# Kernel tuning notes

Measured on AMD Instinct MI355X. Metric: run time of the kernel, lower is better.

The kernel has to match this reference:

```python
import jax, jax.numpy as jnp
import numpy as np

EPS = 1e-5
NUM_HEADS = 8


def _ln(x, g, b):
    m = x.mean(-1, keepdims=True)
    v = jnp.mean((x - m) ** 2, -1, keepdims=True)
    return (x - m) * jax.lax.rsqrt(v + EPS) * g + b


def _bn(x, g, b, m, v):  # eval-mode BatchNorm2d on NCHW
    sh = (1, -1, 1, 1)
    return (x - m.reshape(sh)) * jax.lax.rsqrt(v.reshape(sh) + EPS) * g.reshape(sh) + b.reshape(sh)


def _conv3x3(x, w):
    return jax.lax.conv_general_dilated(x, w, (1, 1), 'SAME', dimension_numbers=('NCHW', 'OIHW', 'NCHW'))


def _gelu(x):
    return jax.nn.gelu(x, approximate=False)  # torch nn.GELU default (erf)


def _attention(x, w_qkv, temperature, w_proj):
    # XCiT-style cross-covariance (channel) attention
    B, N, C = x.shape
    h = NUM_HEADS
    d = C // h
    qkv = (x @ w_qkv.T).reshape(B, N, 3, h, d)
    qkv = jnp.transpose(qkv, (2, 0, 3, 4, 1))  # [3, B, h, d, N]
    q, k, v = qkv[0], qkv[1], qkv[2]
    q = q / jnp.maximum(jnp.linalg.norm(q, axis=-1, keepdims=True), 1e-12)
    k = k / jnp.maximum(jnp.linalg.norm(k, axis=-1, keepdims=True), 1e-12)
    attn = jnp.einsum('bhdn,bhen->bhde', q, k) * temperature[None, :, None, None]
    attn = jax.nn.softmax(attn, axis=-1)  # [B, h, d, d]
    out = jnp.einsum('bhde,bhen->bhdn', attn, v)
    out = jnp.transpose(out, (0, 3, 1, 2)).reshape(B, N, C)
    return out @ w_proj.T


def _forward(x, ln1_g, ln1_b, w_qkv, temperature, w_proj, gamma1,
             ln2_g, ln2_b, mlp_w1, bn1_g, bn1_b, bn1_m, bn1_v,
             mlp_w2, bn2_g, bn2_b, bn2_m, bn2_v, gamma2,
             ln3_g, ln3_b, pconv1, pbn_g, pbn_b, pbn_m, pbn_v, pconv2, gamma3,
             H, W):
    B, N, C = x.shape
    # --- Attention residual block ---
    z = _attention(_ln(x, ln1_g, ln1_b), w_qkv, temperature, w_proj)
    x = x + gamma1 * z
    # --- ConvMlp residual block (1x1 convs + eval BN) ---
    y = _ln(x, ln2_g, ln2_b)
    y = jnp.transpose(y, (0, 2, 1)).reshape(B, C, H, W)
    y = _bn(jnp.einsum('oc,bchw->bohw', mlp_w1, y), bn1_g, bn1_b, bn1_m, bn1_v)
    y = _gelu(y)
    y = _bn(jnp.einsum('oc,bchw->bohw', mlp_w2, y), bn2_g, bn2_b, bn2_m, bn2_v)
    y = jnp.transpose(y.reshape(B, C, N), (0, 2, 1))
    x = x + gamma2 * y
    # --- Projection residual block (3x3 conv + BN + GELU + 3x3 conv) ---
    p = _ln(x, ln3_g, ln3_b)
    p = jnp.transpose(p, (0, 2, 1)).reshape(B, C, H, W)
    p = _conv3x3(p, pconv1)
    p = _gelu(_bn(p, pbn_g, pbn_b, pbn_m, pbn_v))
    p = _conv3x3(p, pconv2)
    p = jnp.transpose(p.reshape(B, C, N), (0, 2, 1))
    x = x + gamma3 * p
    return x


def setup_inputs() -> dict:
    key = jax.random.key(0)
    B, H, W, C, MR = 16, 48, 48, 384, 2
    N = H * W
    C2 = C * MR
    ks = jax.random.split(key, 12)
    nrm = lambda k, sh, s: (jax.random.normal(k, sh) * s).astype(jnp.float32)
    INIT_VALUES = 1e-4  # ResidualBlock default gamma init
    return {
        'x': nrm(ks[0], (B, N, C), 1.0),
        'ln1_g': jnp.ones((C,), jnp.float32), 'ln1_b': jnp.zeros((C,), jnp.float32),
        'w_qkv': nrm(ks[1], (3 * C, C), C ** -0.5),
        'temperature': jnp.ones((NUM_HEADS,), jnp.float32),
        'w_proj': nrm(ks[2], (C, C), C ** -0.5),
        'gamma1': jnp.full((C,), INIT_VALUES, jnp.float32),
        'ln2_g': jnp.ones((C,), jnp.float32), 'ln2_b': jnp.zeros((C,), jnp.float32),
        'mlp_w1': nrm(ks[3], (C2, C), C ** -0.5),
        'bn1_g': jnp.ones((C2,), jnp.float32), 'bn1_b': jnp.zeros((C2,), jnp.float32),
        'bn1_m': nrm(ks[4], (C2,), 0.1), 'bn1_v': jnp.ones((C2,), jnp.float32),
        'mlp_w2': nrm(ks[5], (C, C2), C2 ** -0.5),
        'bn2_g': jnp.ones((C,), jnp.float32), 'bn2_b': jnp.zeros((C,), jnp.float32),
        'bn2_m': nrm(ks[6], (C,), 0.1), 'bn2_v': jnp.ones((C,), jnp.float32),
        'gamma2': jnp.full((C,), INIT_VALUES, jnp.float32),
        'ln3_g': jnp.ones((C,), jnp.float32), 'ln3_b': jnp.zeros((C,), jnp.float32),
        'pconv1': nrm(ks[7], (C, C, 3, 3), (9 * C) ** -0.5),
        'pbn_g': jnp.ones((C,), jnp.float32), 'pbn_b': jnp.zeros((C,), jnp.float32),
        'pbn_m': nrm(ks[8], (C,), 0.1), 'pbn_v': jnp.ones((C,), jnp.float32),
        'pconv2': nrm(ks[9], (C, C, 3, 3), (9 * C) ** -0.5),
        'gamma3': jnp.full((C,), INIT_VALUES, jnp.float32),
        'H': H, 'W': W,
    }


def reference(x, ln1_g, ln1_b, w_qkv, temperature, w_proj, gamma1,
              ln2_g, ln2_b, mlp_w1, bn1_g, bn1_b, bn1_m, bn1_v,
              mlp_w2, bn2_g, bn2_b, bn2_m, bn2_v, gamma2,
              ln3_g, ln3_b, pconv1, pbn_g, pbn_b, pbn_m, pbn_v, pconv2, gamma3,
              H, W):
    out = _forward(x, ln1_g, ln1_b, w_qkv, temperature, w_proj, gamma1,
                   ln2_g, ln2_b, mlp_w1, bn1_g, bn1_b, bn1_m, bn1_v,
                   mlp_w2, bn2_g, bn2_b, bn2_m, bn2_v, gamma2,
                   ln3_g, ln3_b, pconv1, pbn_g, pbn_b, pbn_m, pbn_v, pconv2, gamma3,
                   H, W)
    return (out, H, W)
```

## Files before the change

### kernel.cpp

```cpp
#include <hip/hip_runtime.h>
#include <hip/hip_bf16.h>

typedef unsigned short u16;
typedef __attribute__((ext_vector_type(8))) short short8;
typedef __attribute__((ext_vector_type(4))) float floatx4;

#define LN_EPS 1e-5f

__device__ __forceinline__ float bf2f(u16 u) {
    unsigned int i = ((unsigned int)u) << 16;
    float f; __builtin_memcpy(&f, &i, 4); return f;
}
__device__ __forceinline__ u16 f2bf(float f) {
    __hip_bfloat16 h = __float2bfloat16(f);
    u16 u; __builtin_memcpy(&u, &h, 2); return u;
}

__device__ __forceinline__ void gl_lds16(const u16* g, u16* l) {
    __builtin_amdgcn_global_load_lds(
        (const __attribute__((address_space(1))) void*)(const void*)g,
        (__attribute__((address_space(3))) void*)(void*)l,
        16, 0, 0);
}

__global__ void cvt_f2b_kernel(const float* __restrict__ in, u16* __restrict__ out, int n4) {
    int i = blockIdx.x * blockDim.x + threadIdx.x;
    if (i < n4) {
        float4 f = ((const float4*)in)[i];
        ((ushort4*)out)[i] = make_ushort4(f2bf(f.x), f2bf(f.y), f2bf(f.z), f2bf(f.w));
    }
}

__global__ void zero_kernel(u16* __restrict__ p, int n) {
    int i = blockIdx.x * blockDim.x + threadIdx.x;
    if (i < n) p[i] = 0;
}

__global__ void zero_f32_kernel(float* __restrict__ p, int n) {
    int i = blockIdx.x * blockDim.x + threadIdx.x;
    if (i < n) p[i] = 0.f;
}

__global__ __launch_bounds__(64)
void ln_kernel(const float* __restrict__ xf, const float* __restrict__ g,
               const float* __restrict__ b, u16* __restrict__ out) {
    const int row = blockIdx.x;
    const int lane = threadIdx.x;
    const float* xr = xf + (size_t)row * 384;
    float v[6], s = 0.f, s2 = 0.f;
#pragma unroll
    for (int i = 0; i < 6; ++i) { v[i] = xr[lane + i * 64]; s += v[i]; s2 += v[i] * v[i]; }
#pragma unroll
    for (int off = 32; off; off >>= 1) { s += __shfl_xor(s, off); s2 += __shfl_xor(s2, off); }
    float mean = s * (1.0f / 384.0f);
    float var  = s2 * (1.0f / 384.0f) - mean * mean;
    float rstd = rsqrtf(var + LN_EPS);
    u16* orow = out + (size_t)row * 384;
#pragma unroll
    for (int i = 0; i < 6; ++i) {
        int c = lane + i * 64;
        orow[c] = f2bf((v[i] - mean) * rstd * g[c] + b[c]);
    }
}

template<int ACONV, int EPI>
__global__ __launch_bounds__(256, 2)
void gemm_nt(const u16* __restrict__ A, const u16* __restrict__ Bm,
             int M, int N, int K,
             u16* __restrict__ Obf, int ldo,
             float* __restrict__ xf, float* __restrict__ ofb, const float* __restrict__ xin,
             const float* __restrict__ bn_g, const float* __restrict__ bn_b,
             const float* __restrict__ bn_m, const float* __restrict__ bn_v,
             const float* __restrict__ gamma, const u16* __restrict__ zp) {
    __shared__ u16 As[2][128 * 64];
    __shared__ u16 Bs[2][128 * 64];

    const int tid = threadIdx.x;
    const int gx = gridDim.x;
    const int g  = blockIdx.y * gx + blockIdx.x;
    const int G  = gx * gridDim.y;
    int L = g;
    if ((G & 7) == 0) L = (g & 7) * (G >> 3) + (g >> 3);
    const int n0 = (L % gx) * 128;
    const int m0 = (L / gx) * 128;

    const int lane  = tid & 63;
    const int wave  = tid >> 6;
    const int wm    = (wave >> 1) * 64;
    const int wn    = (wave & 1) * 64;
    const int fr    = lane & 15;
    const int klane = lane >> 4;

    int arow[4], brow[4];
#pragma unroll
    for (int i = 0; i < 4; ++i) {
        arow[i] = (wm + i * 16 + fr) * 64;
        brow[i] = (wn + i * 16 + fr) * 64;
    }
    int csw[2];
#pragma unroll
    for (int kh = 0; kh < 2; ++kh) csw[kh] = ((((kh << 2) + klane) ^ (fr & 7)) << 3);

    int sdst[4];
    int ssc[4];
    const u16 *sa[4], *sb[4];
    int ay[4], ax[4];
    const u16* img = nullptr;
#pragma unroll
    for (int q = 0; q < 4; ++q) {
        int ci  = q * 256 + tid;
        int row = ci >> 3;
        int c   = ci & 7;
        ssc[q]  = ((c ^ (row & 7)) << 3);
        sdst[q] = (q * 256 + wave * 64) << 3;
        sb[q]   = Bm + (size_t)(n0 + row) * K + ssc[q];
        if (ACONV == 0) {
            sa[q] = A + (size_t)(m0 + row) * K + ssc[q];
        } else {
            int nl = (m0 % 2304) + row;
            ay[q] = nl / 48;
            ax[q] = nl - ay[q] * 48;
        }
    }
    if (ACONV == 1) img = A + (size_t)(m0 / 2304) * 2304 * 384;

    int scnt = 0, sjj = 0;
    const int NT = K / 64;

    auto STAGE = [&](int d) {
        if (ACONV == 1) {
            if (scnt == 0) {
                int t3 = sjj / 3;
                int dy = t3 - 1, dx = sjj - t3 * 3 - 1;
                ++sjj;
#pragma unroll
                for (int q = 0; q < 4; ++q) {
                    int yy = ay[q] + dy, xx = ax[q] + dx;
                    bool v = ((unsigned)yy < 48u) & ((unsigned)xx < 48u);
                    sa[q] = (v ? img + (size_t)(yy * 48 + xx) * 384 : zp) + ssc[q];
                }
            }
            scnt = (scnt == 5) ? 0 : scnt + 1;
        }
        u16* la = &As[d][0];
        u16* lb = &Bs[d][0];
#pragma unroll
        for (int q = 0; q < 4; ++q) { gl_lds16(sa[q], la + sdst[q]); sa[q] += 64; }
#pragma unroll
        for (int q = 0; q < 4; ++q) { gl_lds16(sb[q], lb + sdst[q]); sb[q] += 64; }
    };

    floatx4 acc[4][4];
#pragma unroll
    for (int i = 0; i < 4; ++i)
#pragma unroll
        for (int j = 0; j < 4; ++j) acc[i][j] = (floatx4){0.f, 0.f, 0.f, 0.f};

    STAGE(0);
    STAGE(1);
    asm volatile("s_waitcnt vmcnt(8)" ::: "memory");
    __builtin_amdgcn_s_barrier();
    asm volatile("" ::: "memory");

    int cur = 0;
    for (int t = 0; t < NT; ++t) {
        const u16* Ab = &As[cur][0];
        const u16* Bb = &Bs[cur][0];
#pragma unroll
        for (int kh = 0; kh < 2; ++kh) {
            short8 af[4], bfr[4];
#pragma unroll
            for (int i = 0; i < 4; ++i) af[i]  = *(const short8*)(Ab + arow[i] + csw[kh]);
#pragma unroll
            for (int j = 0; j < 4; ++j) bfr[j] = *(const short8*)(Bb + brow[j] + csw[kh]);
#pragma unroll
            for (int i = 0; i < 4; ++i)
#pragma unroll
                for (int j = 0; j < 4; ++j)
                    acc[i][j] = __builtin_amdgcn_mfma_f32_16x16x32_bf16(af[i], bfr[j], acc[i][j], 0, 0, 0);
        }
        asm volatile("s_waitcnt lgkmcnt(0)" ::: "memory");
        __builtin_amdgcn_s_barrier();
        asm volatile("" ::: "memory");
        if (t + 2 < NT) {
            STAGE(cur);
            asm volatile("s_waitcnt vmcnt(8)" ::: "memory");
        } else {
            asm volatile("s_waitcnt vmcnt(0)" ::: "memory");
        }
        __builtin_amdgcn_sched_barrier(0);
        __builtin_amdgcn_s_barrier();
        asm volatile("" ::: "memory");
        cur ^= 1;
    }

    const int quad4 = (lane >> 4) * 4;
#pragma unroll
    for (int j = 0; j < 4; ++j) {
        int col = n0 + wn + j * 16 + fr;
        float bscale = 0.f, bshift = 0.f, gam = 0.f;
        if (EPI == 1 || EPI == 2) {
            bscale = bn_g[col] * rsqrtf(bn_v[col] + LN_EPS);
            bshift = bn_b[col] - bn_m[col] * bscale;
        }
        if (EPI >= 2) gam = gamma[col];
#pragma unroll
        for (int i = 0; i < 4; ++i) {
#pragma unroll
            for (int r = 0; r < 4; ++r) {
                int row = m0 + wm + i * 16 + quad4 + r;
                float v = acc[i][j][r];
                if (EPI == 0) {
                    Obf[(size_t)row * ldo + col] = f2bf(v);
                } else if (EPI == 1) {
                    float t = v * bscale + bshift;
                    t = 0.5f * t * (1.0f + erff(t * 0.70710678118654752f));
                    Obf[(size_t)row * ldo + col] = f2bf(t);
                } else if (EPI == 2) {
                    float t = v * bscale + bshift;
                    xf[(size_t)row * N + col] += gam * t;
                } else if (EPI == 3) {
                    xf[(size_t)row * N + col] += gam * v;
                } else if (EPI == 4) {
                    ofb[(size_t)row * N + col] = xf[(size_t)row * N + col] + gam * v;
                } else {
                    xf[(size_t)row * N + col] = xin[(size_t)row * N + col] + gam * v;
                }
            }
        }
    }
}

__global__ __launch_bounds__(256)
void gram_kernel(const u16* __restrict__ qkv, float* __restrict__ Sacc,
                 float* __restrict__ nrm2) {
    const int bh = blockIdx.y;
    const int b = bh >> 3, h = bh & 7;
    const int tid = threadIdx.x;
    __shared__ float qsf[64][48];
    __shared__ float ksf[64][48];

    float acc9[3][3];
#pragma unroll
    for (int i = 0; i < 3; ++i)
#pragma unroll
        for (int j = 0; j < 3; ++j) acc9[i][j] = 0.f;
    float qn2 = 0.f, kn2 = 0.f;

    const int qoff = h * 48;
    const int koff = 384 + h * 48;
    const int d0 = (tid >> 4) * 3;
    const int e0 = (tid & 15) * 3;
    const int nbase = blockIdx.x * 128;

    for (int c = 0; c < 2; ++c) {
        const int n0 = nbase + c * 64;
#pragma unroll
        for (int it = 0; it < 6; ++it) {
            int chunk = tid + it * 256;
            int mat = chunk >= 768 ? 1 : 0;
            int rem = chunk - mat * 768;
            int nn = rem / 12, u = rem - nn * 12;
            ushort4 raw = *(const ushort4*)(qkv + (size_t)(b * 2304 + n0 + nn) * 1152 +
                                            (mat ? koff : qoff) + u * 4);
            float4 f = make_float4(bf2f(raw.x), bf2f(raw.y), bf2f(raw.z), bf2f(raw.w));
            if (mat) *(float4*)&ksf[nn][u * 4] = f;
            else     *(float4*)&qsf[nn][u * 4] = f;
        }
        __syncthreads();
#pragma unroll 4
        for (int nn = 0; nn < 64; ++nn) {
            float q0 = qsf[nn][d0], q1 = qsf[nn][d0 + 1], q2 = qsf[nn][d0 + 2];
            float k0v = ksf[nn][e0], k1v = ksf[nn][e0 + 1], k2v = ksf[nn][e0 + 2];
            acc9[0][0] += q0 * k0v; acc9[0][1] += q0 * k1v; acc9[0][2] += q0 * k2v;
            acc9[1][0] += q1 * k0v; acc9[1][1] += q1 * k1v; acc9[1][2] += q1 * k2v;
            acc9[2][0] += q2 * k0v; acc9[2][1] += q2 * k1v; acc9[2][2] += q2 * k2v;
        }
        if (tid < 48) {
            for (int nn = 0; nn < 64; ++nn) { float q = qsf[nn][tid]; qn2 += q * q; }
        } else if (tid >= 128 && tid < 176) {
            int e = tid - 128;
            for (int nn = 0; nn < 64; ++nn) { float k = ksf[nn][e]; kn2 += k * k; }
        }
        __syncthreads();
    }

    float* Sb = Sacc + (size_t)bh * 2304;
#pragma unroll
    for (int i = 0; i < 3; ++i)
#pragma unroll
        for (int j = 0; j < 3; ++j)
            atomicAdd(&Sb[(d0 + i) * 48 + e0 + j], acc9[i][j]);
    if (tid < 48) atomicAdd(&nrm2[bh * 96 + tid], qn2);
    else if (tid >= 128 && tid < 176) atomicAdd(&nrm2[bh * 96 + 48 + (tid - 128)], kn2);
}

__global__ __launch_bounds__(256)
void attn_fin_kernel(const float* __restrict__ Sacc, const float* __restrict__ nrm2,
                     const float* __restrict__ temp, float* __restrict__ attnb) {
    const int bh = blockIdx.x;
    const int h = bh & 7;
    const int tid = threadIdx.x;
    __shared__ float S[48][49];
    __shared__ float qns[48], kns[48];

    const float* Sb = Sacc + (size_t)bh * 2304;
    for (int i = tid; i < 2304; i += 256) {
        int d = i / 48, e = i - d * 48;
        S[d][e] = Sb[i];
    }
    if (tid < 48)      qns[tid]      = fmaxf(sqrtf(nrm2[bh * 96 + tid]), 1e-12f);
    else if (tid < 96) kns[tid - 48] = fmaxf(sqrtf(nrm2[bh * 96 + tid]), 1e-12f);
    __syncthreads();

    if (tid < 48) {
        float tf = temp[h] / qns[tid];
        float mx = -1e30f;
        for (int e = 0; e < 48; ++e) {
            float t = S[tid][e] * tf / kns[e];
            S[tid][e] = t;
            mx = fmaxf(mx, t);
        }
        float sum = 0.f;
        for (int e = 0; e < 48; ++e) { float t = __expf(S[tid][e] - mx); S[tid][e] = t; sum += t; }
        float inv = 1.0f / sum;
        float* dst = attnb + ((size_t)bh * 48 + tid) * 48;
        for (int e = 0; e < 48; ++e) dst[e] = S[tid][e] * inv;
    }
}

__global__ __launch_bounds__(256)
void attnout_kernel(const u16* __restrict__ qkv, const float* __restrict__ attnb,
                    u16* __restrict__ z) {
    const int r0 = blockIdx.x * 64;
    const int h  = blockIdx.y;
    const int b  = r0 / 2304;
    const int tid = threadIdx.x;
    __shared__ float A[48][49];
    __shared__ float vsf[64][48];

    const float* asrc = attnb + (size_t)(b * 8 + h) * 2304;
    for (int i = tid; i < 2304; i += 256) {
        int d = i / 48, e = i - d * 48;
        A[d][e] = asrc[i];
    }
    const int voff = 768 + h * 48;
    for (int i = tid; i < 768; i += 256) {
        int nn = i / 12, u = i - nn * 12;
        ushort4 raw = *(const ushort4*)(qkv + (size_t)(r0 + nn) * 1152 + voff + u * 4);
        float4 f = make_float4(bf2f(raw.x), bf2f(raw.y), bf2f(raw.z), bf2f(raw.w));
        *(float4*)&vsf[nn][u * 4] = f;
    }
    __syncthreads();

    const int rr0 = (tid >> 4) * 4;
    const int d0  = (tid & 15) * 3;
    float acc[4][3];
#pragma unroll
    for (int r = 0; r < 4; ++r)
#pragma unroll
        for (int j = 0; j < 3; ++j) acc[r][j] = 0.f;

#pragma unroll 4
    for (int e = 0; e < 48; ++e) {
        float a0 = A[d0][e], a1 = A[d0 + 1][e], a2 = A[d0 + 2][e];
#pragma unroll
        for (int r = 0; r < 4; ++r) {
            float vv = vsf[rr0 + r][e];
            acc[r][0] += a0 * vv; acc[r][1] += a1 * vv; acc[r][2] += a2 * vv;
        }
    }
#pragma unroll
    for (int r = 0; r < 4; ++r)
#pragma unroll
        for (int j = 0; j < 3; ++j)
            z[(size_t)(r0 + rr0 + r) * 384 + h * 48 + d0 + j] = f2bf(acc[r][j]);
}

__global__ void reorder_w_kernel(const float* __restrict__ w, u16* __restrict__ wr, int n) {
    int i = blockIdx.x * blockDim.x + threadIdx.x;
    if (i < n) {
        int o = i / 3456, rem = i - o * 3456;
        int j = rem / 384, c = rem - j * 384;
        wr[i] = f2bf(w[(size_t)(o * 384 + c) * 9 + j]);
    }
}

__global__ void tail_kernel(const int* __restrict__ Hp, const int* __restrict__ Wp,
                            float* __restrict__ out, size_t base, int n_extra) {
    if (threadIdx.x == 0) {
        if (n_extra >= 1) out[base]     = (float)Hp[0];
        if (n_extra >= 2) out[base + 1] = (float)Wp[0];
    }
}

extern "C" void kernel_launch(void* const* d_in, const int* in_sizes, int n_in,
                              void* d_out, int out_size, void* d_ws, size_t ws_size,
                              hipStream_t stream) {
    const float* x      = (const float*)d_in[0];
    const float* ln1_g  = (const float*)d_in[1];
    const float* ln1_b  = (const float*)d_in[2];
    const float* w_qkv  = (const float*)d_in[3];
    const float* temp   = (const float*)d_in[4];
    const float* w_proj = (const float*)d_in[5];
    const float* gamma1 = (const float*)d_in[6];
    const float* ln2_g  = (const float*)d_in[7];
    const float* ln2_b  = (const float*)d_in[8];
    const float* mlp_w1 = (const float*)d_in[9];
    const float* bn1_g  = (const float*)d_in[10];
    const float* bn1_b  = (const float*)d_in[11];
    const float* bn1_m  = (const float*)d_in[12];
    const float* bn1_v  = (const float*)d_in[13];
    const float* mlp_w2 = (const float*)d_in[14];
    const float* bn2_g  = (const float*)d_in[15];
    const float* bn2_b  = (const float*)d_in[16];
    const float* bn2_m  = (const float*)d_in[17];
    const float* bn2_v  = (const float*)d_in[18];
    const float* gamma2 = (const float*)d_in[19];
    const float* ln3_g  = (const float*)d_in[20];
    const float* ln3_b  = (const float*)d_in[21];
    const float* pconv1 = (const float*)d_in[22];
    const float* pbn_g  = (const float*)d_in[23];
    const float* pbn_b  = (const float*)d_in[24];
    const float* pbn_m  = (const float*)d_in[25];
    const float* pbn_v  = (const float*)d_in[26];
    const float* pconv2 = (const float*)d_in[27];
    const float* gamma3 = (const float*)d_in[28];
    const int* Hp = (const int*)d_in[29];
    const int* Wp = (const int*)d_in[30];

    const int M = 36864, C = 384, C2 = 768, NQKV = 1152, KC = 3456;
    const size_t NBNC = (size_t)M * C;

    const size_t SZ_XF  = NBNC * 4;
    const size_t SZ_LN  = NBNC * 2;
    const size_t SZ_BIG = (size_t)M * NQKV * 2;
    const size_t SZ_P3  = SZ_LN;
    const size_t SZ_W   = (size_t)C * KC * 2;
    if (ws_size < SZ_XF + SZ_LN + SZ_BIG + SZ_P3 + 2 * SZ_W) return;

    char* ws = (char*)d_ws;
    float* xf     = (float*)ws;
    u16*   lnbuf  = (u16*)(ws + SZ_XF);
    u16*   big    = (u16*)(ws + SZ_XF + SZ_LN);
    char*  p3     = ws + SZ_XF + SZ_LN + SZ_BIG;
    float* attnb  = (float*)p3;
    u16*   wqkvb  = (u16*)(p3 + 1179648);
    u16*   wprojb = (u16*)(p3 + 1179648 + 884736);
    u16*   w1b    = (u16*)(p3 + 1179648 + 884736 + 294912);
    u16*   w2b    = (u16*)(p3 + 1179648 + 884736 + 294912 + 589824);
    float* Sacc   = (float*)(p3 + 3538944);
    float* nrm2   = (float*)(p3 + 3538944 + 1179648);
    u16*   convbf = (u16*)p3;
    u16*   w1r    = (u16*)(p3 + SZ_P3);
    u16*   w2r    = (u16*)(p3 + SZ_P3 + SZ_W);
    u16*   zp     = big;

    const int n_extra = out_size - (int)NBNC;

    cvt_f2b_kernel<<<(NQKV * C / 4 + 255) / 256, 256, 0, stream>>>(w_qkv, wqkvb, NQKV * C / 4);
    cvt_f2b_kernel<<<(C * C / 4 + 255) / 256, 256, 0, stream>>>(w_proj, wprojb, C * C / 4);
    cvt_f2b_kernel<<<(C2 * C / 4 + 255) / 256, 256, 0, stream>>>(mlp_w1, w1b, C2 * C / 4);
    cvt_f2b_kernel<<<(C * C2 / 4 + 255) / 256, 256, 0, stream>>>(mlp_w2, w2b, C * C2 / 4);
    zero_f32_kernel<<<(128 * 2304 + 128 * 96 + 255) / 256, 256, 0, stream>>>(
        Sacc, 128 * 2304 + 128 * 96);

    ln_kernel<<<M, 64, 0, stream>>>(x, ln1_g, ln1_b, lnbuf);
    gemm_nt<0, 0><<<dim3(NQKV / 128, M / 128), 256, 0, stream>>>(
        lnbuf, wqkvb, M, NQKV, C, big, NQKV, nullptr, nullptr, nullptr,
        nullptr, nullptr, nullptr, nullptr, nullptr, nullptr);
    gram_kernel<<<dim3(18, 128), 256, 0, stream>>>(big, Sacc, nrm2);
    attn_fin_kernel<<<128, 256, 0, stream>>>(Sacc, nrm2, temp, attnb);
    attnout_kernel<<<dim3(M / 64, 8), 256, 0, stream>>>(big, attnb, lnbuf);
    gemm_nt<0, 5><<<dim3(C / 128, M / 128), 256, 0, stream>>>(
        lnbuf, wprojb, M, C, C, nullptr, 0, xf, nullptr, x,
        nullptr, nullptr, nullptr, nullptr, gamma1, nullptr);

    ln_kernel<<<M, 64, 0, stream>>>(xf, ln2_g, ln2_b, lnbuf);
    gemm_nt<0, 1><<<dim3(C2 / 128, M / 128), 256, 0, stream>>>(
        lnbuf, w1b, M, C2, C, big, C2, nullptr, nullptr, nullptr,
        bn1_g, bn1_b, bn1_m, bn1_v, nullptr, nullptr);
    gemm_nt<0, 2><<<dim3(C / 128, M / 128), 256, 0, stream>>>(
        big, w2b, M, C, C2, nullptr, 0, xf, nullptr, nullptr,
        bn2_g, bn2_b, bn2_m, bn2_v, gamma2, nullptr);

    ln_kernel<<<M, 64, 0, stream>>>(xf, ln3_g, ln3_b, lnbuf);
    reorder_w_kernel<<<(C * KC + 255) / 256, 256, 0, stream>>>(pconv1, w1r, C * KC);
    reorder_w_kernel<<<(C * KC + 255) / 256, 256, 0, stream>>>(pconv2, w2r, C * KC);
    zero_kernel<<<8, 256, 0, stream>>>(zp, 2048);
    gemm_nt<1, 1><<<dim3(C / 128, M / 128), 256, 0, stream>>>(
        lnbuf, w1r, M, C, KC, convbf, C, nullptr, nullptr, nullptr,
        pbn_g, pbn_b, pbn_m, pbn_v, nullptr, zp);
    gemm_nt<1, 4><<<dim3(C / 128, M / 128), 256, 0, stream>>>(
        convbf, w2r, M, C, KC, nullptr, 0, xf, (float*)d_out, nullptr,
        nullptr, nullptr, nullptr, nullptr, gamma3, zp);

    tail_kernel<<<1, 64, 0, stream>>>(Hp, Wp, (float*)d_out, NBNC, n_extra);
}
```

Measured before the change: 805.7 us.

## Enlarge GEMM tile to 512x128 with eight waves and MFMA priority boost

Every GEMM/conv kernel now uses 512-thread blocks computing 512x128 output tiles. Each wave owns 64 rows by all 128 columns, so B fragments are shared across the block and A per-wave work doubles. This cuts B reloads and the block count, at the cost of more LDS (160KB double-buffered), more accumulator registers, and fewer blocks, which may hurt occupancy and tail balance at this problem size. It also brackets the MFMA loop with s_setprio and adds sched barriers, and lets conv tiles span image boundaries.

Measured after the change: 833.5 us. +3.4%, slower.

```diff
diff --git a/kernel.cpp b/kernel.cpp
--- a/kernel.cpp
+++ b/kernel.cpp
@@ -64,7 +64,7 @@
 }
 
 template<int ACONV, int EPI>
-__global__ __launch_bounds__(256, 2)
+__global__ __launch_bounds__(512, 2)
 void gemm_nt(const u16* __restrict__ A, const u16* __restrict__ Bm,
              int M, int N, int K,
              u16* __restrict__ Obf, int ldo,
@@ -72,7 +72,7 @@
              const float* __restrict__ bn_g, const float* __restrict__ bn_b,
              const float* __restrict__ bn_m, const float* __restrict__ bn_v,
              const float* __restrict__ gamma, const u16* __restrict__ zp) {
-    __shared__ u16 As[2][128 * 64];
+    __shared__ u16 As[2][512 * 64];
     __shared__ u16 Bs[2][128 * 64];
 
     const int tid = threadIdx.x;
@@ -82,47 +82,45 @@
     int L = g;
     if ((G & 7) == 0) L = (g & 7) * (G >> 3) + (g >> 3);
     const int n0 = (L % gx) * 128;
-    const int m0 = (L / gx) * 128;
+    const int m0 = (L / gx) * 512;
 
     const int lane  = tid & 63;
     const int wave  = tid >> 6;
-    const int wm    = (wave >> 1) * 64;
-    const int wn    = (wave & 1) * 64;
+    const int wm    = wave * 64;
     const int fr    = lane & 15;
     const int klane = lane >> 4;
 
-    int arow[4], brow[4];
-#pragma unroll
-    for (int i = 0; i < 4; ++i) {
-        arow[i] = (wm + i * 16 + fr) * 64;
-        brow[i] = (wn + i * 16 + fr) * 64;
-    }
+    int arow[4], brow[8];
+#pragma unroll
+    for (int i = 0; i < 4; ++i) arow[i] = (wm + i * 16 + fr) * 64;
+#pragma unroll
+    for (int j = 0; j < 8; ++j) brow[j] = (j * 16 + fr) * 64;
     int csw[2];
 #pragma unroll
     for (int kh = 0; kh < 2; ++kh) csw[kh] = ((((kh << 2) + klane) ^ (fr & 7)) << 3);
 
-    int sdst[4];
-    int ssc[4];
-    const u16 *sa[4], *sb[4];
-    int ay[4], ax[4];
-    const u16* img = nullptr;
-#pragma unroll
-    for (int q = 0; q < 4; ++q) {
-        int ci  = q * 256 + tid;
-        int row = ci >> 3;
-        int c   = ci & 7;
-        ssc[q]  = ((c ^ (row & 7)) << 3);
-        sdst[q] = (q * 256 + wave * 64) << 3;
-        sb[q]   = Bm + (size_t)(n0 + row) * K + ssc[q];
+    const int srow = tid >> 3;
+    const int ssc  = (((tid & 7) ^ (srow & 7)) << 3);
+    const u16 *sa[8], *sb[2];
+    const u16* imgq[8];
+    int ay[8], ax[8];
+#pragma unroll
+    for (int q = 0; q < 8; ++q) {
+        int r = q * 64 + srow;
         if (ACONV == 0) {
-            sa[q] = A + (size_t)(m0 + row) * K + ssc[q];
+            sa[q] = A + (size_t)(m0 + r) * K + ssc;
         } else {
-            int nl = (m0 % 2304) + row;
+            int nA = m0 + r;
+            int bi = nA / 2304;
+            int nl = nA - bi * 2304;
             ay[q] = nl / 48;
             ax[q] = nl - ay[q] * 48;
-        }
-    }
-    if (ACONV == 1) img = A + (size_t)(m0 / 2304) * 2304 * 384;
+            imgq[q] = A + (size_t)bi * 2304 * 384;
+        }
+    }
+#pragma unroll
+    for (int q = 0; q < 2; ++q)
+        sb[q] = Bm + (size_t)(n0 + q * 64 + srow) * K + ssc;
 
     int scnt = 0, sjj = 0;
     const int NT = K / 64;
@@ -134,10 +132,10 @@
                 int dy = t3 - 1, dx = sjj - t3 * 3 - 1;
                 ++sjj;
 #pragma unroll
-                for (int q = 0; q < 4; ++q) {
+                for (int q = 0; q < 8; ++q) {
                     int yy = ay[q] + dy, xx = ax[q] + dx;
                     bool v = ((unsigned)yy < 48u) & ((unsigned)xx < 48u);
-                    sa[q] = (v ? img + (size_t)(yy * 48 + xx) * 384 : zp) + ssc[q];
+                    sa[q] = (v ? imgq[q] + (size_t)(yy * 48 + xx) * 384 : zp) + ssc;
                 }
             }
             scnt = (scnt == 5) ? 0 : scnt + 1;
@@ -145,20 +143,21 @@
         u16* la = &As[d][0];
         u16* lb = &Bs[d][0];
 #pragma unroll
-        for (int q = 0; q < 4; ++q) { gl_lds16(sa[q], la + sdst[q]); sa[q] += 64; }
-#pragma unroll
-        for (int q = 0; q < 4; ++q) { gl_lds16(sb[q], lb + sdst[q]); sb[q] += 64; }
+        for (int q = 0; q < 8; ++q) { gl_lds16(sa[q], la + ((q * 512 + wave * 64) << 3)); sa[q] += 64; }
+#pragma unroll
+        for (int q = 0; q < 2; ++q) { gl_lds16(sb[q], lb + ((q * 512 + wave * 64) << 3)); sb[q] += 64; }
     };
 
-    floatx4 acc[4][4];
+    floatx4 acc[4][8];
 #pragma unroll
     for (int i = 0; i < 4; ++i)
 #pragma unroll
-        for (int j = 0; j < 4; ++j) acc[i][j] = (floatx4){0.f, 0.f, 0.f, 0.f};
+        for (int j = 0; j < 8; ++j) acc[i][j] = (floatx4){0.f, 0.f, 0.f, 0.f};
 
     STAGE(0);
     STAGE(1);
-    asm volatile("s_waitcnt vmcnt(8)" ::: "memory");
+    asm volatile("s_waitcnt vmcnt(10)" ::: "memory");
+    __builtin_amdgcn_sched_barrier(0);
     __builtin_amdgcn_s_barrier();
     asm volatile("" ::: "memory");
 
@@ -168,23 +167,26 @@
         const u16* Bb = &Bs[cur][0];
 #pragma unroll
         for (int kh = 0; kh < 2; ++kh) {
-            short8 af[4], bfr[4];
+            short8 af[4], bfr[8];
 #pragma unroll
             for (int i = 0; i < 4; ++i) af[i]  = *(const short8*)(Ab + arow[i] + csw[kh]);
 #pragma unroll
-            for (int j = 0; j < 4; ++j) bfr[j] = *(const short8*)(Bb + brow[j] + csw[kh]);
+            for (int j = 0; j < 8; ++j) bfr[j] = *(const short8*)(Bb + brow[j] + csw[kh]);
+            __builtin_amdgcn_s_setprio(1);
 #pragma unroll
             for (int i = 0; i < 4; ++i)
 #pragma unroll
-                for (int j = 0; j < 4; ++j)
+                for (int j = 0; j < 8; ++j)
                     acc[i][j] = __builtin_amdgcn_mfma_f32_16x16x32_bf16(af[i], bfr[j], acc[i][j], 0, 0, 0);
+            __builtin_amdgcn_s_setprio(0);
         }
         asm volatile("s_waitcnt lgkmcnt(0)" ::: "memory");
+        __builtin_amdgcn_sched_barrier(0);
         __builtin_amdgcn_s_barrier();
         asm volatile("" ::: "memory");
         if (t + 2 < NT) {
             STAGE(cur);
-            asm volatile("s_waitcnt vmcnt(8)" ::: "memory");
+            asm volatile("s_waitcnt vmcnt(10)" ::: "memory");
         } else {
             asm volatile("s_waitcnt vmcnt(0)" ::: "memory");
         }
@@ -196,8 +198,8 @@
 
     const int quad4 = (lane >> 4) * 4;
 #pragma unroll
-    for (int j = 0; j < 4; ++j) {
-        int col = n0 + wn + j * 16 + fr;
+    for (int j = 0; j < 8; ++j) {
+        int col = n0 + j * 16 + fr;
         float bscale = 0.f, bshift = 0.f, gam = 0.f;
         if (EPI == 1 || EPI == 2) {
             bscale = bn_g[col] * rsqrtf(bn_v[col] + LN_EPS);
@@ -466,21 +468,21 @@
         Sacc, 128 * 2304 + 128 * 96);
 
     ln_kernel<<<M, 64, 0, stream>>>(x, ln1_g, ln1_b, lnbuf);
-    gemm_nt<0, 0><<<dim3(NQKV / 128, M / 128), 256, 0, stream>>>(
+    gemm_nt<0, 0><<<dim3(NQKV / 128, M / 512), 512, 0, stream>>>(
         lnbuf, wqkvb, M, NQKV, C, big, NQKV, nullptr, nullptr, nullptr,
         nullptr, nullptr, nullptr, nullptr, nullptr, nullptr);
     gram_kernel<<<dim3(18, 128), 256, 0, stream>>>(big, Sacc, nrm2);
     attn_fin_kernel<<<128, 256, 0, stream>>>(Sacc, nrm2, temp, attnb);
     attnout_kernel<<<dim3(M / 64, 8), 256, 0, stream>>>(big, attnb, lnbuf);
-    gemm_nt<0, 5><<<dim3(C / 128, M / 128), 256, 0, stream>>>(
+    gemm_nt<0, 5><<<dim3(C / 128, M / 512), 512, 0, stream>>>(
         lnbuf, wprojb, M, C, C, nullptr, 0, xf, nullptr, x,
         nullptr, nullptr, nullptr, nullptr, gamma1, nullptr);
 
     ln_kernel<<<M, 64, 0, stream>>>(xf, ln2_g, ln2_b, lnbuf);
-    gemm_nt<0, 1><<<dim3(C2 / 128, M / 128), 256, 0, stream>>>(
+    gemm_nt<0, 1><<<dim3(C2 / 128, M / 512), 512, 0, stream>>>(
         lnbuf, w1b, M, C2, C, big, C2, nullptr, nullptr, nullptr,
         bn1_g, bn1_b, bn1_m, bn1_v, nullptr, nullptr);
-    gemm_nt<0, 2><<<dim3(C / 128, M / 128), 256, 0, stream>>>(
+    gemm_nt<0, 2><<<dim3(C / 128, M / 512), 512, 0, stream>>>(
         big, w2b, M, C, C2, nullptr, 0, xf, nullptr, nullptr,
         bn2_g, bn2_b, bn2_m, bn2_v, gamma2, nullptr);
 
@@ -488,10 +490,10 @@
     reorder_w_kernel<<<(C * KC + 255) / 256, 256, 0, stream>>>(pconv1, w1r, C * KC);
     reorder_w_kernel<<<(C * KC + 255) / 256, 256, 0, stream>>>(pconv2, w2r, C * KC);
     zero_kernel<<<8, 256, 0, stream>>>(zp, 2048);
-    gemm_nt<1, 1><<<dim3(C / 128, M / 128), 256, 0, stream>>>(
+    gemm_nt<1, 1><<<dim3(C / 128, M / 512), 512, 0, stream>>>(
         lnbuf, w1r, M, C, KC, convbf, C, nullptr, nullptr, nullptr,
         pbn_g, pbn_b, pbn_m, pbn_v, nullptr, zp);
-    gemm_nt<1, 4><<<dim3(C / 128, M / 128), 256, 0, stream>>>(
+    gemm_nt<1, 4><<<dim3(C / 128, M / 512), 512, 0, stream>>>(
         convbf, w2r, M, C, KC, nullptr, 0, xf, (float*)d_out, nullptr,
         nullptr, nullptr, nullptr, nullptr, gamma3, zp);
 
```

## Switch GEMM operands and activations from bf16 to fp8 e4m3 MFMA

Applied to the files above, without the earlier changes.

Converts weights, layernorm outputs, attention outputs and GELU intermediates to fp8 (e4m3) and runs all GEMMs, including the implicit 3x3 convolutions, with the fp8 16x16x32 MFMA instead of bf16. The LDS tiles shrink by half, the staging loop and swizzle are rewritten for byte elements, and launch bounds rise to allow more resident blocks. This aims to halve operand memory traffic and raise matrix throughput, at the cost of much lower precision that may break accuracy tolerances.

After: 743.0 us. 7.8% less time.

```diff
diff --git a/kernel.cpp b/kernel.cpp
--- a/kernel.cpp
+++ b/kernel.cpp
@@ -2,7 +2,7 @@
 #include <hip/hip_bf16.h>
 
 typedef unsigned short u16;
-typedef __attribute__((ext_vector_type(8))) short short8;
+typedef unsigned char  u8;
 typedef __attribute__((ext_vector_type(4))) float floatx4;
 
 #define LN_EPS 1e-5f
@@ -15,19 +15,24 @@
     __hip_bfloat16 h = __float2bfloat16(f);
     u16 u; __builtin_memcpy(&u, &h, 2); return u;
 }
-
-__device__ __forceinline__ void gl_lds16(const u16* g, u16* l) {
+__device__ __forceinline__ u8 f2e4(float f) {
+    int p = __builtin_amdgcn_cvt_pk_fp8_f32(f, f, 0, false);
+    return (u8)(p & 0xff);
+}
+
+__device__ __forceinline__ void gl_lds16(const u8* g, u8* l) {
     __builtin_amdgcn_global_load_lds(
         (const __attribute__((address_space(1))) void*)(const void*)g,
         (__attribute__((address_space(3))) void*)(void*)l,
         16, 0, 0);
 }
 
-__global__ void cvt_f2b_kernel(const float* __restrict__ in, u16* __restrict__ out, int n4) {
+__global__ void cvt_f2e4_kernel(const float* __restrict__ in, u8* __restrict__ out, int n4) {
     int i = blockIdx.x * blockDim.x + threadIdx.x;
     if (i < n4) {
         float4 f = ((const float4*)in)[i];
-        ((ushort4*)out)[i] = make_ushort4(f2bf(f.x), f2bf(f.y), f2bf(f.z), f2bf(f.w));
+        uchar4 o; o.x = f2e4(f.x); o.y = f2e4(f.y); o.z = f2e4(f.z); o.w = f2e4(f.w);
+        ((uchar4*)out)[i] = o;
     }
 }
 
@@ -43,7 +48,7 @@
 
 __global__ __launch_bounds__(64)
 void ln_kernel(const float* __restrict__ xf, const float* __restrict__ g,
-               const float* __restrict__ b, u16* __restrict__ out) {
+               const float* __restrict__ b, u8* __restrict__ out) {
     const int row = blockIdx.x;
     const int lane = threadIdx.x;
     const float* xr = xf + (size_t)row * 384;
@@ -55,25 +60,25 @@
     float mean = s * (1.0f / 384.0f);
     float var  = s2 * (1.0f / 384.0f) - mean * mean;
     float rstd = rsqrtf(var + LN_EPS);
-    u16* orow = out + (size_t)row * 384;
+    u8* orow = out + (size_t)row * 384;
 #pragma unroll
     for (int i = 0; i < 6; ++i) {
         int c = lane + i * 64;
-        orow[c] = f2bf((v[i] - mean) * rstd * g[c] + b[c]);
+        orow[c] = f2e4((v[i] - mean) * rstd * g[c] + b[c]);
     }
 }
 
 template<int ACONV, int EPI>
-__global__ __launch_bounds__(256, 2)
-void gemm_nt(const u16* __restrict__ A, const u16* __restrict__ Bm,
+__global__ __launch_bounds__(256, 4)
+void gemm_nt(const u8* __restrict__ A, const u8* __restrict__ Bm,
              int M, int N, int K,
              u16* __restrict__ Obf, int ldo,
              float* __restrict__ xf, float* __restrict__ ofb, const float* __restrict__ xin,
              const float* __restrict__ bn_g, const float* __restrict__ bn_b,
              const float* __restrict__ bn_m, const float* __restrict__ bn_v,
-             const float* __restrict__ gamma, const u16* __restrict__ zp) {
-    __shared__ u16 As[2][128 * 64];
-    __shared__ u16 Bs[2][128 * 64];
+             const float* __restrict__ gamma, const u8* __restrict__ zp) {
+    __shared__ u8 As[2][128 * 64];
+    __shared__ u8 Bs[2][128 * 64];
 
     const int tid = threadIdx.x;
     const int gx = gridDim.x;
@@ -99,30 +104,29 @@
     }
     int csw[2];
 #pragma unroll
-    for (int kh = 0; kh < 2; ++kh) csw[kh] = ((((kh << 2) + klane) ^ (fr & 7)) << 3);
-
-    int sdst[4];
-    int ssc[4];
-    const u16 *sa[4], *sb[4];
-    int ay[4], ax[4];
-    const u16* img = nullptr;
-#pragma unroll
-    for (int q = 0; q < 4; ++q) {
-        int ci  = q * 256 + tid;
-        int row = ci >> 3;
-        int c   = ci & 7;
-        ssc[q]  = ((c ^ (row & 7)) << 3);
-        sdst[q] = (q * 256 + wave * 64) << 3;
-        sb[q]   = Bm + (size_t)(n0 + row) * K + ssc[q];
+    for (int kh = 0; kh < 2; ++kh)
+        csw[kh] = ((((kh << 1) + (klane >> 1)) ^ (fr & 3)) << 4) + ((klane & 1) << 3);
+
+    const int srow = tid >> 2;
+    const int ssc  = (((tid & 3) ^ (srow & 3)) << 4);
+    const u8 *sa[2], *sb[2];
+    const u8* imgq[2];
+    int ay[2], ax[2];
+#pragma unroll
+    for (int q = 0; q < 2; ++q) {
+        int r = q * 64 + srow;
         if (ACONV == 0) {
-            sa[q] = A + (size_t)(m0 + row) * K + ssc[q];
+            sa[q] = A + (size_t)(m0 + r) * K + ssc;
         } else {
-            int nl = (m0 % 2304) + row;
+            int nA = m0 + r;
+            int bi = nA / 2304;
+            int nl = nA - bi * 2304;
             ay[q] = nl / 48;
             ax[q] = nl - ay[q] * 48;
-        }
-    }
-    if (ACONV == 1) img = A + (size_t)(m0 / 2304) * 2304 * 384;
+            imgq[q] = A + (size_t)bi * 2304 * 384;
+        }
+        sb[q] = Bm + (size_t)(n0 + q * 64 + srow) * K + ssc;
+    }
 
     int scnt = 0, sjj = 0;
     const int NT = K / 64;
@@ -134,20 +138,20 @@
                 int dy = t3 - 1, dx = sjj - t3 * 3 - 1;
                 ++sjj;
 #pragma unroll
-                for (int q = 0; q < 4; ++q) {
+                for (int q = 0; q < 2; ++q) {
                     int yy = ay[q] + dy, xx = ax[q] + dx;
                     bool v = ((unsigned)yy < 48u) & ((unsigned)xx < 48u);
-                    sa[q] = (v ? img + (size_t)(yy * 48 + xx) * 384 : zp) + ssc[q];
+                    sa[q] = (v ? imgq[q] + (size_t)(yy * 48 + xx) * 384 : zp) + ssc;
                 }
             }
             scnt = (scnt == 5) ? 0 : scnt + 1;
         }
-        u16* la = &As[d][0];
-        u16* lb = &Bs[d][0];
-#pragma unroll
-        for (int q = 0; q < 4; ++q) { gl_lds16(sa[q], la + sdst[q]); sa[q] += 64; }
-#pragma unroll
-        for (int q = 0; q < 4; ++q) { gl_lds16(sb[q], lb + sdst[q]); sb[q] += 64; }
+        u8* la = &As[d][0];
+        u8* lb = &Bs[d][0];
+        gl_lds16(sa[0], la + ((wave * 64) << 4));        sa[0] += 64;
+        gl_lds16(sa[1], la + ((256 + wave * 64) << 4));  sa[1] += 64;
+        gl_lds16(sb[0], lb + ((wave * 64) << 4));        sb[0] += 64;
+        gl_lds16(sb[1], lb + ((256 + wave * 64) << 4));  sb[1] += 64;
     };
 
     floatx4 acc[4][4];
@@ -158,33 +162,33 @@
 
     STAGE(0);
     STAGE(1);
-    asm volatile("s_waitcnt vmcnt(8)" ::: "memory");
+    asm volatile("s_waitcnt vmcnt(4)" ::: "memory");
     __builtin_amdgcn_s_barrier();
     asm volatile("" ::: "memory");
 
     int cur = 0;
     for (int t = 0; t < NT; ++t) {
-        const u16* Ab = &As[cur][0];
-        const u16* Bb = &Bs[cur][0];
+        const u8* Ab = &As[cur][0];
+        const u8* Bb = &Bs[cur][0];
 #pragma unroll
         for (int kh = 0; kh < 2; ++kh) {
-            short8 af[4], bfr[4];
-#pragma unroll
-            for (int i = 0; i < 4; ++i) af[i]  = *(const short8*)(Ab + arow[i] + csw[kh]);
-#pragma unroll
-            for (int j = 0; j < 4; ++j) bfr[j] = *(const short8*)(Bb + brow[j] + csw[kh]);
+            long af[4], bfr[4];
+#pragma unroll
+            for (int i = 0; i < 4; ++i) af[i]  = *(const long*)(Ab + arow[i] + csw[kh]);
+#pragma unroll
+            for (int j = 0; j < 4; ++j) bfr[j] = *(const long*)(Bb + brow[j] + csw[kh]);
 #pragma unroll
             for (int i = 0; i < 4; ++i)
 #pragma unroll
                 for (int j = 0; j < 4; ++j)
-                    acc[i][j] = __builtin_amdgcn_mfma_f32_16x16x32_bf16(af[i], bfr[j], acc[i][j], 0, 0, 0);
+                    acc[i][j] = __builtin_amdgcn_mfma_f32_16x16x32_fp8_fp8(af[i], bfr[j], acc[i][j], 0, 0, 0);
         }
         asm volatile("s_waitcnt lgkmcnt(0)" ::: "memory");
         __builtin_amdgcn_s_barrier();
         asm volatile("" ::: "memory");
         if (t + 2 < NT) {
             STAGE(cur);
-            asm volatile("s_waitcnt vmcnt(8)" ::: "memory");
+            asm volatile("s_waitcnt vmcnt(4)" ::: "memory");
         } else {
             asm volatile("s_waitcnt vmcnt(0)" ::: "memory");
         }
@@ -215,7 +219,7 @@
                 } else if (EPI == 1) {
                     float t = v * bscale + bshift;
                     t = 0.5f * t * (1.0f + erff(t * 0.70710678118654752f));
-                    Obf[(size_t)row * ldo + col] = f2bf(t);
+                    ((u8*)Obf)[(size_t)row * ldo + col] = f2e4(t);
                 } else if (EPI == 2) {
                     float t = v * bscale + bshift;
                     xf[(size_t)row * N + col] += gam * t;
@@ -331,7 +335,7 @@
 
 __global__ __launch_bounds__(256)
 void attnout_kernel(const u16* __restrict__ qkv, const float* __restrict__ attnb,
-                    u16* __restrict__ z) {
+                    u8* __restrict__ z) {
     const int r0 = blockIdx.x * 64;
     const int h  = blockIdx.y;
     const int b  = r0 / 2304;
@@ -374,15 +378,15 @@
     for (int r = 0; r < 4; ++r)
 #pragma unroll
         for (int j = 0; j < 3; ++j)
-            z[(size_t)(r0 + rr0 + r) * 384 + h * 48 + d0 + j] = f2bf(acc[r][j]);
-}
-
-__global__ void reorder_w_kernel(const float* __restrict__ w, u16* __restrict__ wr, int n) {
+            z[(size_t)(r0 + rr0 + r) * 384 + h * 48 + d0 + j] = f2e4(acc[r][j]);
+}
+
+__global__ void reorder_w_kernel(const float* __restrict__ w, u8* __restrict__ wr, int n) {
     int i = blockIdx.x * blockDim.x + threadIdx.x;
     if (i < n) {
         int o = i / 3456, rem = i - o * 3456;
         int j = rem / 384, c = rem - j * 384;
-        wr[i] = f2bf(w[(size_t)(o * 384 + c) * 9 + j]);
+        wr[i] = f2e4(w[(size_t)(o * 384 + c) * 9 + j]);
     }
 }
 
@@ -441,27 +445,27 @@
 
     char* ws = (char*)d_ws;
     float* xf     = (float*)ws;
-    u16*   lnbuf  = (u16*)(ws + SZ_XF);
+    u8*    lnbuf  = (u8*)(ws + SZ_XF);
     u16*   big    = (u16*)(ws + SZ_XF + SZ_LN);
     char*  p3     = ws + SZ_XF + SZ_LN + SZ_BIG;
     float* attnb  = (float*)p3;
-    u16*   wqkvb  = (u16*)(p3 + 1179648);
-    u16*   wprojb = (u16*)(p3 + 1179648 + 884736);
-    u16*   w1b    = (u16*)(p3 + 1179648 + 884736 + 294912);
-    u16*   w2b    = (u16*)(p3 + 1179648 + 884736 + 294912 + 589824);
+    u8*    wqkvb  = (u8*)(p3 + 1179648);
+    u8*    wprojb = (u8*)(p3 + 1179648 + 884736);
+    u8*    w1b    = (u8*)(p3 + 1179648 + 884736 + 294912);
+    u8*    w2b    = (u8*)(p3 + 1179648 + 884736 + 294912 + 589824);
     float* Sacc   = (float*)(p3 + 3538944);
     float* nrm2   = (float*)(p3 + 3538944 + 1179648);
-    u16*   convbf = (u16*)p3;
-    u16*   w1r    = (u16*)(p3 + SZ_P3);
-    u16*   w2r    = (u16*)(p3 + SZ_P3 + SZ_W);
-    u16*   zp     = big;
+    u8*    convbf = (u8*)p3;
+    u8*    w1r    = (u8*)(p3 + SZ_P3);
+    u8*    w2r    = (u8*)(p3 + SZ_P3 + SZ_W);
+    u8*    zp     = (u8*)big;
 
     const int n_extra = out_size - (int)NBNC;
 
-    cvt_f2b_kernel<<<(NQKV * C / 4 + 255) / 256, 256, 0, stream>>>(w_qkv, wqkvb, NQKV * C / 4);
-    cvt_f2b_kernel<<<(C * C / 4 + 255) / 256, 256, 0, stream>>>(w_proj, wprojb, C * C / 4);
-    cvt_f2b_kernel<<<(C2 * C / 4 + 255) / 256, 256, 0, stream>>>(mlp_w1, w1b, C2 * C / 4);
-    cvt_f2b_kernel<<<(C * C2 / 4 + 255) / 256, 256, 0, stream>>>(mlp_w2, w2b, C * C2 / 4);
+    cvt_f2e4_kernel<<<(NQKV * C / 4 + 255) / 256, 256, 0, stream>>>(w_qkv, wqkvb, NQKV * C / 4);
+    cvt_f2e4_kernel<<<(C * C / 4 + 255) / 256, 256, 0, stream>>>(w_proj, wprojb, C * C / 4);
+    cvt_f2e4_kernel<<<(C2 * C / 4 + 255) / 256, 256, 0, stream>>>(mlp_w1, w1b, C2 * C / 4);
+    cvt_f2e4_kernel<<<(C * C2 / 4 + 255) / 256, 256, 0, stream>>>(mlp_w2, w2b, C * C2 / 4);
     zero_f32_kernel<<<(128 * 2304 + 128 * 96 + 255) / 256, 256, 0, stream>>>(
         Sacc, 128 * 2304 + 128 * 96);
 
@@ -478,18 +482,18 @@
 
     ln_kernel<<<M, 64, 0, stream>>>(xf, ln2_g, ln2_b, lnbuf);
     gemm_nt<0, 1><<<dim3(C2 / 128, M / 128), 256, 0, stream>>>(
-        lnbuf, w1b, M, C2, C, big, C2, nullptr, nullptr, nullptr,
+        lnbuf, w1b, M, C2, C, (u16*)big, C2, nullptr, nullptr, nullptr,
         bn1_g, bn1_b, bn1_m, bn1_v, nullptr, nullptr);
     gemm_nt<0, 2><<<dim3(C / 128, M / 128), 256, 0, stream>>>(
-        big, w2b, M, C, C2, nullptr, 0, xf, nullptr, nullptr,
+        (u8*)big, w2b, M, C, C2, nullptr, 0, xf, nullptr, nullptr,
         bn2_g, bn2_b, bn2_m, bn2_v, gamma2, nullptr);
 
     ln_kernel<<<M, 64, 0, stream>>>(xf, ln3_g, ln3_b, lnbuf);
     reorder_w_kernel<<<(C * KC + 255) / 256, 256, 0, stream>>>(pconv1, w1r, C * KC);
     reorder_w_kernel<<<(C * KC + 255) / 256, 256, 0, stream>>>(pconv2, w2r, C * KC);
-    zero_kernel<<<8, 256, 0, stream>>>(zp, 2048);
+    zero_kernel<<<8, 256, 0, stream>>>((u16*)zp, 2048);
     gemm_nt<1, 1><<<dim3(C / 128, M / 128), 256, 0, stream>>>(
-        lnbuf, w1r, M, C, KC, convbf, C, nullptr, nullptr, nullptr,
+        lnbuf, w1r, M, C, KC, (u16*)convbf, C, nullptr, nullptr, nullptr,
         pbn_g, pbn_b, pbn_m, pbn_v, nullptr, zp);
     gemm_nt<1, 4><<<dim3(C / 128, M / 128), 256, 0, stream>>>(
         convbf, w2r, M, C, KC, nullptr, 0, xf, (float*)d_out, nullptr,
```
